# Kernel optimization log

Measured on AMD Instinct MI355X. Metric: run time of the kernel, lower is better.

## Reference

```python
import jax, jax.numpy as jnp
import numpy as np

B, T, D, H = 8, 512, 1024, 16
DH = D // H  # per-head feature dim (64)


def setup_inputs() -> dict:
    key = jax.random.key(0)
    ks = jax.random.split(key, 10)
    s = 1.0 / np.sqrt(DH)
    inp = {
        "X_data": jax.random.normal(ks[0], (B, T, D), dtype=jnp.float32),
        "mask": jnp.ones((B, T), dtype=jnp.int32),
        # per-head Q/K/V projections (each SelfAttention has its own d_h x d_h weights)
        "Wq": jax.random.normal(ks[1], (H, DH, DH), dtype=jnp.float32) * s,
        "bq": jnp.zeros((H, DH), dtype=jnp.float32),
        "Wk": jax.random.normal(ks[2], (H, DH, DH), dtype=jnp.float32) * s,
        "bk": jnp.zeros((H, DH), dtype=jnp.float32),
        "Wv": jax.random.normal(ks[3], (H, DH, DH), dtype=jnp.float32) * s,
        "bv": jnp.zeros((H, DH), dtype=jnp.float32),
        # AttentionFusion: linear on concatenated head outputs -> len_feature_new
        "Wf": jax.random.normal(ks[4], (D, D), dtype=jnp.float32) * (1.0 / np.sqrt(D)),
        "bf": jnp.zeros((D,), dtype=jnp.float32),
    }
    return inp


def reference(X_data, mask, Wq, bq, Wk, bk, Wv, bv, Wf, bf):
    # Split features into heads: [B, T, H, DH] (equal partitions since D % H == 0)
    Xh = X_data.reshape(B, T, H, DH)
    # Batched per-head projections (replaces the Python loop over heads)
    Q = jnp.einsum("bthd,hde->bhte", Xh, Wq) + bq[None, :, None, :]
    K = jnp.einsum("bthd,hde->bhte", Xh, Wk) + bk[None, :, None, :]
    V = jnp.einsum("bthd,hde->bhte", Xh, Wv) + bv[None, :, None, :]
    scale = 1.0 / jnp.sqrt(jnp.asarray(DH, dtype=Q.dtype))
    scores = jnp.einsum("bhqe,bhke->bhqk", Q, K) * scale  # [B, H, T, T]
    scores = jnp.where(mask[:, None, None, :] > 0, scores, jnp.asarray(-1e9, scores.dtype))
    att = jax.nn.softmax(scores, axis=-1)
    out = jnp.einsum("bhqk,bhke->bhqe", att, V)  # [B, H, T, DH]
    # Concatenate heads (same order as the per-head loop) and fuse
    out = out.transpose(0, 2, 1, 3).reshape(B, T, D)
    fused = out @ Wf + bf  # AttentionFusion linear
    return fused
```

## Files before the change

kernel.cpp:

```cpp
#include <hip/hip_runtime.h>
#include <math.h>

#define B 8
#define T 512
#define D 1024
#define H 16
#define DH 64

typedef __bf16 bf16;
typedef __attribute__((ext_vector_type(8))) __bf16 bf16x8;
typedef __attribute__((ext_vector_type(4))) float f32x4;

__device__ __forceinline__ void gld16(const void* g, void* l) {
    __builtin_amdgcn_global_load_lds(
        (const __attribute__((address_space(1))) void*)g,
        (__attribute__((address_space(3))) void*)l, 16, 0, 0);
}


__global__ __launch_bounds__(256) void prep_w(
    const float* __restrict__ Wq, const float* __restrict__ Wk,
    const float* __restrict__ Wv, const float* __restrict__ Wf,
    bf16* __restrict__ WqT, bf16* __restrict__ WkT,
    bf16* __restrict__ WvT, bf16* __restrict__ WfT)
{
    __shared__ bf16 Ts[64 * 72];
    const int blk = blockIdx.x, tid = threadIdx.x;
    if (blk < 48) {
        const int m = blk >> 4, h = blk & 15;
        const float* src = (m == 0 ? Wq : (m == 1 ? Wk : Wv)) + h * 4096;
        bf16* dst = (m == 0 ? WqT : (m == 1 ? WkT : WvT)) + h * 4096;
        for (int i = tid; i < 1024; i += 256) {
            const int d = i >> 4, eq = (i & 15) * 4;
            const float4 w = *(const float4*)(src + d * 64 + eq);
            Ts[(eq + 0) * 72 + d] = (bf16)w.x; Ts[(eq + 1) * 72 + d] = (bf16)w.y;
            Ts[(eq + 2) * 72 + d] = (bf16)w.z; Ts[(eq + 3) * 72 + d] = (bf16)w.w;
        }
        __syncthreads();
        for (int i = tid; i < 512; i += 256) {
            const int e = i >> 3, kc = (i & 7) * 8;
            *(bf16x8*)(dst + e * 64 + kc) = *(const bf16x8*)&Ts[e * 72 + kc];
        }
    } else {
        const int ti = blk - 48, k0 = (ti >> 4) * 64, n0 = (ti & 15) * 64;
        for (int i = tid; i < 1024; i += 256) {
            const int k = i >> 4, nq = (i & 15) * 4;
            const float4 w = *(const float4*)(Wf + (size_t)(k0 + k) * D + n0 + nq);
            Ts[(nq + 0) * 72 + k] = (bf16)w.x; Ts[(nq + 1) * 72 + k] = (bf16)w.y;
            Ts[(nq + 2) * 72 + k] = (bf16)w.z; Ts[(nq + 3) * 72 + k] = (bf16)w.w;
        }
        __syncthreads();
        for (int i = tid; i < 512; i += 256) {
            const int n = i >> 3, kc = (i & 7) * 8;
            *(bf16x8*)(WfT + (size_t)(n0 + n) * D + k0 + kc) = *(const bf16x8*)&Ts[n * 72 + kc];
        }
    }
}

__global__ __launch_bounds__(256, 3) void qkv_attn(
    const float* __restrict__ X, const int* __restrict__ mask,
    const bf16* __restrict__ WqT, const bf16* __restrict__ WkT,
    const bf16* __restrict__ WvT,
    const float* __restrict__ bq, const float* __restrict__ bk,
    const float* __restrict__ bv,
    bf16* __restrict__ Ob)
{
    __shared__ __align__(16) char smem[53504];
    bf16* Wks = (bf16*)(smem);
    bf16* Wvs = (bf16*)(smem + 8192);
    bf16* Ks  = (bf16*)(smem + 16384);
    bf16* Vts = (bf16*)(smem + 25600);
    bf16* Pl  = (bf16*)(smem + 34816);
    int*  msk = (int*)(smem + 53248);
    bf16* Wqs   = Ks;
    bf16* Xq    = Vts;
    bf16* Stage = Pl;
    bf16* Xkt   = Pl;
    bf16* Ostage = Pl;

    const int bh = blockIdx.x & 127, q0 = (blockIdx.x >> 7) * 128;
    const int b = bh >> 4, h = bh & 15;
    const int tid = threadIdx.x, wave = tid >> 6, lane = tid & 63;
    const int quad = lane >> 4, l15 = lane & 15;
    const int lr = lane >> 3, lc = lane & 7;
    const int csw = (lc ^ lr) * 8;

    float bqr[4], bkr[4], bvr[4];
#pragma unroll
    for (int nt = 0; nt < 4; ++nt) {
        bqr[nt] = bq[h * DH + nt * 16 + l15];
        bkr[nt] = bk[h * DH + nt * 16 + l15];
        bvr[nt] = bv[h * DH + nt * 16 + l15];
    }

    {
        const int r1 = wave * 16;
#pragma unroll
        for (int j = 0; j < 2; ++j) {
            gld16(WqT + (size_t)h * 4096 + (r1 + j * 8 + lr) * 64 + csw, &Wqs[(r1 + j * 8) * 64]);
            gld16(WkT + (size_t)h * 4096 + (r1 + j * 8 + lr) * 64 + csw, &Wks[(r1 + j * 8) * 64]);
            gld16(WvT + (size_t)h * 4096 + (r1 + j * 8 + lr) * 64 + csw, &Wvs[(r1 + j * 8) * 64]);
        }
    }
    for (int i = tid; i < 1024; i += 256) {
        const int row = i >> 3, c = i & 7;
        const float* src = X + (size_t)(b * T + q0 + row) * D + h * DH + c * 8;
        const float4 x0 = *(const float4*)src;
        const float4 x1 = *(const float4*)(src + 4);
        bf16x8 t;
        t[0] = (bf16)x0.x; t[1] = (bf16)x0.y; t[2] = (bf16)x0.z; t[3] = (bf16)x0.w;
        t[4] = (bf16)x1.x; t[5] = (bf16)x1.y; t[6] = (bf16)x1.z; t[7] = (bf16)x1.w;
        *(bf16x8*)&Xq[row * 64 + ((c ^ (row & 7)) * 8)] = t;
    }
    __syncthreads();

    {
        f32x4 accQ[2][4] = {};
#pragma unroll
        for (int ks = 0; ks < 2; ++ks) {
            bf16x8 af[2], bfr[4];
#pragma unroll
            for (int mt = 0; mt < 2; ++mt) {
                const int row = wave * 32 + mt * 16 + l15;
                af[mt] = *(const bf16x8*)&Xq[row * 64 + (((ks * 4 + quad) ^ (l15 & 7)) * 8)];
            }
#pragma unroll
            for (int nt = 0; nt < 4; ++nt)
                bfr[nt] = *(const bf16x8*)&Wqs[(nt * 16 + l15) * 64 + (((ks * 4 + quad) ^ (l15 & 7)) * 8)];
#pragma unroll
            for (int mt = 0; mt < 2; ++mt)
#pragma unroll
                for (int nt = 0; nt < 4; ++nt)
                    accQ[mt][nt] = __builtin_amdgcn_mfma_f32_16x16x32_bf16(af[mt], bfr[nt], accQ[mt][nt], 0, 0, 0);
        }
        __syncthreads();
#pragma unroll
        for (int mt = 0; mt < 2; ++mt)
#pragma unroll
            for (int nt = 0; nt < 4; ++nt)
#pragma unroll
                for (int reg = 0; reg < 4; ++reg)
                    Stage[(wave * 32 + mt * 16 + quad * 4 + reg) * 72 + nt * 16 + l15] =
                        (bf16)((accQ[mt][nt][reg] + bqr[nt]) * 0.125f);
        __builtin_amdgcn_wave_barrier();
    }
    bf16x8 qf[2][2];
#pragma unroll
    for (int mt = 0; mt < 2; ++mt)
#pragma unroll
        for (int ks = 0; ks < 2; ++ks)
            qf[mt][ks] = *(const bf16x8*)&Stage[(wave * 32 + mt * 16 + l15) * 72 + ks * 32 + quad * 8];

    f32x4 acc[2][4] = {};
    float lst[2][4] = {};

    for (int kt = 0; kt < 8; ++kt) {
        const int k0 = kt * 64;
        __syncthreads();
        if (tid < 64) msk[tid] = mask[(size_t)b * T + k0 + tid];
        {
            const int krow = wave * 16 + (lane >> 2);
            const int c0 = (lane & 3) * 2;
            const float* src = X + (size_t)(b * T + k0 + krow) * D + h * DH + c0 * 8;
            const float4 x0 = *(const float4*)src;
            const float4 x1 = *(const float4*)(src + 4);
            const float4 x2 = *(const float4*)(src + 8);
            const float4 x3 = *(const float4*)(src + 12);
            bf16x8 t0, t1;
            t0[0] = (bf16)x0.x; t0[1] = (bf16)x0.y; t0[2] = (bf16)x0.z; t0[3] = (bf16)x0.w;
            t0[4] = (bf16)x1.x; t0[5] = (bf16)x1.y; t0[6] = (bf16)x1.z; t0[7] = (bf16)x1.w;
            t1[0] = (bf16)x2.x; t1[1] = (bf16)x2.y; t1[2] = (bf16)x2.z; t1[3] = (bf16)x2.w;
            t1[4] = (bf16)x3.x; t1[5] = (bf16)x3.y; t1[6] = (bf16)x3.z; t1[7] = (bf16)x3.w;
            *(bf16x8*)&Xkt[krow * 64 + ((c0 ^ (krow & 7)) * 8)] = t0;
            *(bf16x8*)&Xkt[krow * 64 + (((c0 + 1) ^ (krow & 7)) * 8)] = t1;
        }
        __builtin_amdgcn_wave_barrier();

        {
            bf16x8 afkv[2];
#pragma unroll
            for (int ks = 0; ks < 2; ++ks)
                afkv[ks] = *(const bf16x8*)&Xkt[(wave * 16 + l15) * 64 + (((ks * 4 + quad) ^ (l15 & 7)) * 8)];
            f32x4 accK[4] = {}, accV[4] = {};
#pragma unroll
            for (int ks = 0; ks < 2; ++ks)
#pragma unroll
                for (int nt = 0; nt < 4; ++nt) {
                    const bf16x8 bk8 = *(const bf16x8*)&Wks[(nt * 16 + l15) * 64 + (((ks * 4 + quad) ^ (l15 & 7)) * 8)];
                    accK[nt] = __builtin_amdgcn_mfma_f32_16x16x32_bf16(afkv[ks], bk8, accK[nt], 0, 0, 0);
                    const bf16x8 bv8 = *(const bf16x8*)&Wvs[(nt * 16 + l15) * 64 + (((ks * 4 + quad) ^ (l15 & 7)) * 8)];
                    accV[nt] = __builtin_amdgcn_mfma_f32_16x16x32_bf16(afkv[ks], bv8, accV[nt], 0, 0, 0);
                }
#pragma unroll
            for (int nt = 0; nt < 4; ++nt)
#pragma unroll
                for (int reg = 0; reg < 4; ++reg) {
                    const int key = wave * 16 + quad * 4 + reg;
                    const int e = nt * 16 + l15;
                    Ks[key * 72 + e] = (bf16)(accK[nt][reg] + bkr[nt]);
                    Vts[e * 72 + key] = (bf16)(accV[nt][reg] + bvr[nt]);
                }
        }
        __syncthreads();

        bf16* Plw = Pl + wave * (32 * 72);
        {
            bf16x8 kf[4][2];
#pragma unroll
            for (int nt = 0; nt < 4; ++nt)
#pragma unroll
                for (int ks = 0; ks < 2; ++ks)
                    kf[nt][ks] = *(const bf16x8*)&Ks[(nt * 16 + l15) * 72 + ks * 32 + quad * 8];
            int mv[4];
#pragma unroll
            for (int nt = 0; nt < 4; ++nt) mv[nt] = msk[nt * 16 + l15];
#pragma unroll
            for (int mt = 0; mt < 2; ++mt) {
                f32x4 s[4] = {};
#pragma unroll
                for (int ks = 0; ks < 2; ++ks)
#pragma unroll
                    for (int nt = 0; nt < 4; ++nt)
                        s[nt] = __builtin_amdgcn_mfma_f32_16x16x32_bf16(qf[mt][ks], kf[nt][ks], s[nt], 0, 0, 0);
#pragma unroll
                for (int nt = 0; nt < 4; ++nt)
#pragma unroll
                    for (int reg = 0; reg < 4; ++reg) {
                        const float p = (mv[nt] > 0) ? __expf(s[nt][reg]) : 0.f;
                        lst[mt][reg] += p;
                        Plw[(mt * 16 + quad * 4 + reg) * 72 + nt * 16 + l15] = (bf16)p;
                    }
            }
        }
        __builtin_amdgcn_wave_barrier();

#pragma unroll
        for (int kc = 0; kc < 2; ++kc) {
            const bf16x8 pf0 = *(const bf16x8*)&Plw[(l15) * 72 + kc * 32 + quad * 8];
            const bf16x8 pf1 = *(const bf16x8*)&Plw[(16 + l15) * 72 + kc * 32 + quad * 8];
#pragma unroll
            for (int nt = 0; nt < 4; ++nt) {
                const bf16x8 vf = *(const bf16x8*)&Vts[(nt * 16 + l15) * 72 + kc * 32 + quad * 8];
                acc[0][nt] = __builtin_amdgcn_mfma_f32_16x16x32_bf16(pf0, vf, acc[0][nt], 0, 0, 0);
                acc[1][nt] = __builtin_amdgcn_mfma_f32_16x16x32_bf16(pf1, vf, acc[1][nt], 0, 0, 0);
            }
        }
    }

    __builtin_amdgcn_wave_barrier();
#pragma unroll
    for (int mt = 0; mt < 2; ++mt)
#pragma unroll
        for (int reg = 0; reg < 4; ++reg) {
            float l = lst[mt][reg];
            l += __shfl_xor(l, 1);
            l += __shfl_xor(l, 2);
            l += __shfl_xor(l, 4);
            l += __shfl_xor(l, 8);
            const float inv = 1.f / l;
            const int row = wave * 32 + mt * 16 + quad * 4 + reg;
#pragma unroll
            for (int nt = 0; nt < 4; ++nt)
                Ostage[row * 72 + nt * 16 + l15] = (bf16)(acc[mt][nt][reg] * inv);
        }
    __syncthreads();
    for (int i = tid; i < 1024; i += 256) {
        const int row = i >> 3, c = (i & 7) * 8;
        *(bf16x8*)(Ob + ((size_t)b * T + q0 + row) * D + h * DH + c) =
            *(const bf16x8*)&Ostage[row * 72 + c];
    }
}

__global__ __launch_bounds__(256) void fuse_mfma(
    const bf16* __restrict__ Ob, const bf16* __restrict__ WfT,
    const float* __restrict__ bfv, float* __restrict__ out)
{
    __shared__ bf16 smem[128 * 128 + 64 * 128];
    bf16* As = smem;
    bf16* Bs = smem + 128 * 128;

    const int col0 = blockIdx.x * 64;
    const int row0 = blockIdx.y * 128;
    const int tid = threadIdx.x, wave = tid >> 6, lane = tid & 63;
    const int quad = lane >> 4, l15 = lane & 15;
    const int lr4 = lane >> 4, lc16 = lane & 15;
    const int wm = wave * 32;

    f32x4 acc[2][4] = {};

    for (int k0 = 0; k0 < D; k0 += 128) {
        __syncthreads();
#pragma unroll
        for (int j = 0; j < 8; ++j) {
            const int row = wm + j * 4 + lr4;
            gld16(Ob + (size_t)(row0 + row) * D + k0 + ((lc16 ^ (row & 15)) * 8),
                  &As[(wm + j * 4) * 128]);
        }
#pragma unroll
        for (int j = 0; j < 4; ++j) {
            const int row = wave * 16 + j * 4 + lr4;
            gld16(WfT + (size_t)(col0 + row) * D + k0 + ((lc16 ^ (row & 15)) * 8),
                  &Bs[(wave * 16 + j * 4) * 128]);
        }
        __syncthreads();
#pragma unroll
        for (int ks = 0; ks < 4; ++ks) {
            bf16x8 af[2], bfr[4];
#pragma unroll
            for (int mt = 0; mt < 2; ++mt) {
                const int row = wm + mt * 16 + l15;
                af[mt] = *(const bf16x8*)&As[row * 128 + ((ks * 4 + quad) ^ l15) * 8];
            }
#pragma unroll
            for (int nt = 0; nt < 4; ++nt)
                bfr[nt] = *(const bf16x8*)&Bs[(nt * 16 + l15) * 128 + ((ks * 4 + quad) ^ l15) * 8];
#pragma unroll
            for (int mt = 0; mt < 2; ++mt)
#pragma unroll
                for (int nt = 0; nt < 4; ++nt)
                    acc[mt][nt] = __builtin_amdgcn_mfma_f32_16x16x32_bf16(af[mt], bfr[nt], acc[mt][nt], 0, 0, 0);
        }
    }

    __syncthreads();
    float* Ofs = (float*)smem;
    float bias[4];
#pragma unroll
    for (int nt = 0; nt < 4; ++nt) bias[nt] = bfv[col0 + nt * 16 + l15];
#pragma unroll
    for (int mt = 0; mt < 2; ++mt)
#pragma unroll
        for (int reg = 0; reg < 4; ++reg) {
            const int row = wm + mt * 16 + quad * 4 + reg;
#pragma unroll
            for (int nt = 0; nt < 4; ++nt)
                Ofs[row * 68 + nt * 16 + l15] = acc[mt][nt][reg] + bias[nt];
        }
    __syncthreads();
    for (int i = tid; i < 2048; i += 256) {
        const int row = i >> 4, c = (i & 15) * 4;
        *(float4*)(out + (size_t)(row0 + row) * D + col0 + c) = *(const float4*)&Ofs[row * 68 + c];
    }
}

extern "C" void kernel_launch(void* const* d_in, const int* in_sizes, int n_in,
                              void* d_out, int out_size, void* d_ws, size_t ws_size,
                              hipStream_t stream) {
    const float* X   = (const float*)d_in[0];
    const int* mask  = (const int*)d_in[1];
    const float* Wq  = (const float*)d_in[2];
    const float* bq  = (const float*)d_in[3];
    const float* Wk  = (const float*)d_in[4];
    const float* bk  = (const float*)d_in[5];
    const float* Wv  = (const float*)d_in[6];
    const float* bv  = (const float*)d_in[7];
    const float* Wf  = (const float*)d_in[8];
    const float* bfv = (const float*)d_in[9];
    float* out = (float*)d_out;

    bf16* wsb = (bf16*)d_ws;
    const size_t QN = (size_t)B * H * T * DH;
    bf16* Ob  = wsb;
    bf16* WfT = wsb + QN;
    bf16* WqT = WfT + (size_t)D * D;
    bf16* WkT = WqT + H * DH * DH;
    bf16* WvT = WkT + H * DH * DH;

    prep_w<<<dim3(304), 256, 0, stream>>>(Wq, Wk, Wv, Wf, WqT, WkT, WvT, WfT);
    qkv_attn<<<dim3(512), 256, 0, stream>>>(X, mask, WqT, WkT, WvT, bq, bk, bv, Ob);
    fuse_mfma<<<dim3(D / 64, (B * T) / 128), 256, 0, stream>>>(Ob, WfT, bfv, out);
}
```

Measured before the change: 130.6 us.

## Double-buffer K/V tiles and fusion GEMM stages, prefetch X, use exp2

In the attention kernel, the next 64-row X tile and mask chunk are prefetched into registers while the current tile is processed. K/V and mask are ping-ponged across two shared-memory buffers so one block barrier per iteration can go, and softmax uses exp2f with log2(e) folded into the Q scale. The fusion GEMM switches to 64-wide K stages that are double-buffered with async global-to-LDS loads, so the next stage loads during the current stage's MFMAs. Both kernels grow their LDS footprint and drop to two blocks per CU, trading occupancy for overlap.

```diff
diff --git a/kernel.cpp b/kernel.cpp
--- a/kernel.cpp
+++ b/kernel.cpp
@@ -17,6 +17,8 @@
         (__attribute__((address_space(3))) void*)l, 16, 0, 0);
 }
 
+
+#define EXP2SCALE 1.44269504088896f
 
 __global__ __launch_bounds__(256) void prep_w(
     const float* __restrict__ Wq, const float* __restrict__ Wk,
@@ -57,7 +59,7 @@
     }
 }
 
-__global__ __launch_bounds__(256, 3) void qkv_attn(
+__global__ __launch_bounds__(256, 2) void qkv_attn(
     const float* __restrict__ X, const int* __restrict__ mask,
     const bf16* __restrict__ WqT, const bf16* __restrict__ WkT,
     const bf16* __restrict__ WvT,
@@ -65,17 +67,15 @@
     const float* __restrict__ bv,
     bf16* __restrict__ Ob)
 {
-    __shared__ __align__(16) char smem[53504];
+    __shared__ __align__(16) char smem[80384];
     bf16* Wks = (bf16*)(smem);
     bf16* Wvs = (bf16*)(smem + 8192);
-    bf16* Ks  = (bf16*)(smem + 16384);
-    bf16* Vts = (bf16*)(smem + 25600);
-    bf16* Pl  = (bf16*)(smem + 34816);
-    int*  msk = (int*)(smem + 53248);
-    bf16* Wqs   = Ks;
-    bf16* Xq    = Vts;
+    bf16* Pl  = (bf16*)(smem + 53248);
+    bf16* Xkt = (bf16*)(smem + 71680);
+    int*  msk = (int*)(smem + 79872);
+    bf16* Wqs   = (bf16*)(smem + 16384);
+    bf16* Xq    = Pl;
     bf16* Stage = Pl;
-    bf16* Xkt   = Pl;
     bf16* Ostage = Pl;
 
     const int bh = blockIdx.x & 127, q0 = (blockIdx.x >> 7) * 128;
@@ -85,6 +85,9 @@
     const int lr = lane >> 3, lc = lane & 7;
     const int csw = (lc ^ lr) * 8;
 
+    const int pkrow = wave * 16 + (lane >> 2);
+    const int pc0 = (lane & 3) * 2;
+
     float bqr[4], bkr[4], bvr[4];
 #pragma unroll
     for (int nt = 0; nt < 4; ++nt) {
@@ -92,6 +95,14 @@
         bkr[nt] = bk[h * DH + nt * 16 + l15];
         bvr[nt] = bv[h * DH + nt * 16 + l15];
     }
+
+    float4 px0, px1, px2, px3;
+    {
+        const float* src = X + (size_t)(b * T + pkrow) * D + h * DH + pc0 * 8;
+        px0 = *(const float4*)src; px1 = *(const float4*)(src + 4);
+        px2 = *(const float4*)(src + 8); px3 = *(const float4*)(src + 12);
+    }
+    int mreg = (tid < 64) ? mask[(size_t)b * T + tid] : 0;
 
     {
         const int r1 = wave * 16;
@@ -134,6 +145,7 @@
                     accQ[mt][nt] = __builtin_amdgcn_mfma_f32_16x16x32_bf16(af[mt], bfr[nt], accQ[mt][nt], 0, 0, 0);
         }
         __syncthreads();
+        const float qs = 0.125f * EXP2SCALE;
 #pragma unroll
         for (int mt = 0; mt < 2; ++mt)
 #pragma unroll
@@ -141,7 +153,7 @@
 #pragma unroll
                 for (int reg = 0; reg < 4; ++reg)
                     Stage[(wave * 32 + mt * 16 + quad * 4 + reg) * 72 + nt * 16 + l15] =
-                        (bf16)((accQ[mt][nt][reg] + bqr[nt]) * 0.125f);
+                        (bf16)((accQ[mt][nt][reg] + bqr[nt]) * qs);
         __builtin_amdgcn_wave_barrier();
     }
     bf16x8 qf[2][2];
@@ -155,26 +167,28 @@
     float lst[2][4] = {};
 
     for (int kt = 0; kt < 8; ++kt) {
-        const int k0 = kt * 64;
-        __syncthreads();
-        if (tid < 64) msk[tid] = mask[(size_t)b * T + k0 + tid];
+        const int p = kt & 1;
+        bf16* Ks  = (bf16*)(smem + 16384 + p * 9216);
+        bf16* Vts = (bf16*)(smem + 34816 + p * 9216);
+
         {
-            const int krow = wave * 16 + (lane >> 2);
-            const int c0 = (lane & 3) * 2;
-            const float* src = X + (size_t)(b * T + k0 + krow) * D + h * DH + c0 * 8;
-            const float4 x0 = *(const float4*)src;
-            const float4 x1 = *(const float4*)(src + 4);
-            const float4 x2 = *(const float4*)(src + 8);
-            const float4 x3 = *(const float4*)(src + 12);
             bf16x8 t0, t1;
-            t0[0] = (bf16)x0.x; t0[1] = (bf16)x0.y; t0[2] = (bf16)x0.z; t0[3] = (bf16)x0.w;
-            t0[4] = (bf16)x1.x; t0[5] = (bf16)x1.y; t0[6] = (bf16)x1.z; t0[7] = (bf16)x1.w;
-            t1[0] = (bf16)x2.x; t1[1] = (bf16)x2.y; t1[2] = (bf16)x2.z; t1[3] = (bf16)x2.w;
-            t1[4] = (bf16)x3.x; t1[5] = (bf16)x3.y; t1[6] = (bf16)x3.z; t1[7] = (bf16)x3.w;
-            *(bf16x8*)&Xkt[krow * 64 + ((c0 ^ (krow & 7)) * 8)] = t0;
-            *(bf16x8*)&Xkt[krow * 64 + (((c0 + 1) ^ (krow & 7)) * 8)] = t1;
+            t0[0] = (bf16)px0.x; t0[1] = (bf16)px0.y; t0[2] = (bf16)px0.z; t0[3] = (bf16)px0.w;
+            t0[4] = (bf16)px1.x; t0[5] = (bf16)px1.y; t0[6] = (bf16)px1.z; t0[7] = (bf16)px1.w;
+            t1[0] = (bf16)px2.x; t1[1] = (bf16)px2.y; t1[2] = (bf16)px2.z; t1[3] = (bf16)px2.w;
+            t1[4] = (bf16)px3.x; t1[5] = (bf16)px3.y; t1[6] = (bf16)px3.z; t1[7] = (bf16)px3.w;
+            *(bf16x8*)&Xkt[pkrow * 64 + ((pc0 ^ (pkrow & 7)) * 8)] = t0;
+            *(bf16x8*)&Xkt[pkrow * 64 + (((pc0 + 1) ^ (pkrow & 7)) * 8)] = t1;
+            if (tid < 64) msk[p * 64 + tid] = mreg;
         }
         __builtin_amdgcn_wave_barrier();
+
+        if (kt < 7) {
+            const float* src = X + (size_t)(b * T + (kt + 1) * 64 + pkrow) * D + h * DH + pc0 * 8;
+            px0 = *(const float4*)src; px1 = *(const float4*)(src + 4);
+            px2 = *(const float4*)(src + 8); px3 = *(const float4*)(src + 12);
+            if (tid < 64) mreg = mask[(size_t)b * T + (kt + 1) * 64 + tid];
+        }
 
         {
             bf16x8 afkv[2];
@@ -213,7 +227,7 @@
                     kf[nt][ks] = *(const bf16x8*)&Ks[(nt * 16 + l15) * 72 + ks * 32 + quad * 8];
             int mv[4];
 #pragma unroll
-            for (int nt = 0; nt < 4; ++nt) mv[nt] = msk[nt * 16 + l15];
+            for (int nt = 0; nt < 4; ++nt) mv[nt] = msk[p * 64 + nt * 16 + l15];
 #pragma unroll
             for (int mt = 0; mt < 2; ++mt) {
                 f32x4 s[4] = {};
@@ -226,9 +240,9 @@
                 for (int nt = 0; nt < 4; ++nt)
 #pragma unroll
                     for (int reg = 0; reg < 4; ++reg) {
-                        const float p = (mv[nt] > 0) ? __expf(s[nt][reg]) : 0.f;
-                        lst[mt][reg] += p;
-                        Plw[(mt * 16 + quad * 4 + reg) * 72 + nt * 16 + l15] = (bf16)p;
+                        const float pv = (mv[nt] > 0) ? exp2f(s[nt][reg]) : 0.f;
+                        lst[mt][reg] += pv;
+                        Plw[(mt * 16 + quad * 4 + reg) * 72 + nt * 16 + l15] = (bf16)pv;
                     }
             }
         }
@@ -271,58 +285,66 @@
     }
 }
 
-__global__ __launch_bounds__(256) void fuse_mfma(
+__global__ __launch_bounds__(256, 2) void fuse_mfma(
     const bf16* __restrict__ Ob, const bf16* __restrict__ WfT,
     const float* __restrict__ bfv, float* __restrict__ out)
 {
-    __shared__ bf16 smem[128 * 128 + 64 * 128];
-    bf16* As = smem;
-    bf16* Bs = smem + 128 * 128;
+    __shared__ __align__(16) char smem[49152];
 
     const int col0 = blockIdx.x * 64;
     const int row0 = blockIdx.y * 128;
     const int tid = threadIdx.x, wave = tid >> 6, lane = tid & 63;
     const int quad = lane >> 4, l15 = lane & 15;
-    const int lr4 = lane >> 4, lc16 = lane & 15;
+    const int lr = lane >> 3, lc = lane & 7;
     const int wm = wave * 32;
 
     f32x4 acc[2][4] = {};
 
-    for (int k0 = 0; k0 < D; k0 += 128) {
-        __syncthreads();
-#pragma unroll
-        for (int j = 0; j < 8; ++j) {
-            const int row = wm + j * 4 + lr4;
-            gld16(Ob + (size_t)(row0 + row) * D + k0 + ((lc16 ^ (row & 15)) * 8),
-                  &As[(wm + j * 4) * 128]);
-        }
+    auto stage = [&](int k0, int buf) {
+        bf16* As = (bf16*)(smem + buf * 16384);
+        bf16* Bs = (bf16*)(smem + 32768 + buf * 8192);
 #pragma unroll
         for (int j = 0; j < 4; ++j) {
-            const int row = wave * 16 + j * 4 + lr4;
-            gld16(WfT + (size_t)(col0 + row) * D + k0 + ((lc16 ^ (row & 15)) * 8),
-                  &Bs[(wave * 16 + j * 4) * 128]);
-        }
-        __syncthreads();
-#pragma unroll
-        for (int ks = 0; ks < 4; ++ks) {
+            const int row = wm + j * 8 + lr;
+            gld16(Ob + (size_t)(row0 + row) * D + k0 + ((lc ^ (row & 7)) * 8),
+                  &As[(wm + j * 8) * 64]);
+        }
+#pragma unroll
+        for (int j = 0; j < 2; ++j) {
+            const int row = wave * 16 + j * 8 + lr;
+            gld16(WfT + (size_t)(col0 + row) * D + k0 + ((lc ^ (row & 7)) * 8),
+                  &Bs[(wave * 16 + j * 8) * 64]);
+        }
+    };
+
+    stage(0, 0);
+    __syncthreads();
+
+    for (int i = 0; i < 16; ++i) {
+        const int buf = i & 1;
+        if (i < 15) stage((i + 1) * 64, buf ^ 1);
+        bf16* As = (bf16*)(smem + buf * 16384);
+        bf16* Bs = (bf16*)(smem + 32768 + buf * 8192);
+#pragma unroll
+        for (int ks = 0; ks < 2; ++ks) {
             bf16x8 af[2], bfr[4];
 #pragma unroll
             for (int mt = 0; mt < 2; ++mt) {
                 const int row = wm + mt * 16 + l15;
-                af[mt] = *(const bf16x8*)&As[row * 128 + ((ks * 4 + quad) ^ l15) * 8];
+                af[mt] = *(const bf16x8*)&As[row * 64 + (((ks * 4 + quad) ^ (l15 & 7)) * 8)];
             }
 #pragma unroll
             for (int nt = 0; nt < 4; ++nt)
-                bfr[nt] = *(const bf16x8*)&Bs[(nt * 16 + l15) * 128 + ((ks * 4 + quad) ^ l15) * 8];
+                bfr[nt] = *(const bf16x8*)&Bs[(nt * 16 + l15) * 64 + (((ks * 4 + quad) ^ (l15 & 7)) * 8)];
 #pragma unroll
             for (int mt = 0; mt < 2; ++mt)
 #pragma unroll
                 for (int nt = 0; nt < 4; ++nt)
                     acc[mt][nt] = __builtin_amdgcn_mfma_f32_16x16x32_bf16(af[mt], bfr[nt], acc[mt][nt], 0, 0, 0);
         }
-    }
-
-    __syncthreads();
+        __syncthreads();
+    }
+
     float* Ofs = (float*)smem;
     float bias[4];
 #pragma unroll
```

Result: no change. 128.5 us (-1.6%).
